# Kernel optimization log

Measured on AMD Instinct MI355X. Metric: run time of the kernel, lower is better.

Reference implementation:

```python
import jax, jax.numpy as jnp
import numpy as np
import math

B, L, NH, HD = 2, 2048, 8, 128
C = NH * HD            # hidden size
K = 3                  # short_conv_L
EMB, ORDER = 33, 64    # hyena filter emb_dim / order


def setup_inputs() -> dict:
    key = jax.random.key(0)
    ks = jax.random.split(key, 10)
    f32 = jnp.float32
    return {
        "query_layer": jax.random.normal(ks[0], (L, B, NH, HD), f32),
        "key_layer": jax.random.normal(ks[1], (L, B, NH, HD), f32),
        "value_layer": jax.random.normal(ks[2], (L, B, NH, HD), f32),
        # depthwise short conv params: [3(qkv), C, 1, K] / [3, C]
        "short_conv_weight": jax.random.normal(ks[3], (3, C, 1, K), f32) * 0.3,
        "short_conv_bias": jax.random.normal(ks[4], (3, C), f32) * 0.02,
        # D term of the long conv, shape [head_dim]
        "long_conv_bias": jax.random.normal(ks[5], (HD,), f32) * 0.1,
        # hyena filter MLP (torch Linear convention: W [out, in])
        "lin0_w": jax.random.normal(ks[6], (ORDER, EMB), f32) * (1.0 / np.sqrt(EMB)),
        "lin0_b": jnp.zeros((ORDER,), f32),
        "lin1_w": jax.random.normal(ks[7], (ORDER, ORDER), f32) * (1.0 / np.sqrt(ORDER)),
        "lin1_b": jnp.zeros((ORDER,), f32),
        "lin2_w": jax.random.normal(ks[8], (ORDER, ORDER), f32) * (1.0 / np.sqrt(ORDER)),
        "lin2_b": jnp.zeros((ORDER,), f32),
        "freq": jnp.ones((1, ORDER), f32),  # Sin activation freq (w=1), shared across layers
        "final_w": jax.random.normal(ks[9], (HD, ORDER), f32) * (1.0 / np.sqrt(ORDER)),
        # exponential modulation decay rates, [1,1,HD], as initialized in the module
        "mod_weight": jnp.linspace(math.log(0.01) / 1.5, math.log(0.01) / 0.3, HD,
                                   dtype=f32)[None, None],
    }


def _depthwise_conv(x, w, b):
    # x [B,C,L], w [C,1,K], b [C]; causal: pad K-1 both sides, keep first L
    y = jax.lax.conv_general_dilated(
        x, w, window_strides=(1,), padding=[(K - 1, K - 1)],
        feature_group_count=C, dimension_numbers=("NCH", "OIH", "NCH"))
    return y[..., :L] + b[None, :, None]


def _hyena_filter(lin0_w, lin0_b, lin1_w, lin1_b, lin2_w, lin2_b, freq, final_w, mod_weight):
    t = jnp.linspace(0.0, 1.0, L)[None, :, None]              # [1,L,1]
    bands = (EMB - 1) // 2
    w_ang = 2.0 * jnp.pi * jnp.linspace(0.0, L - 1.0, L) / L  # [L]
    f = jnp.linspace(1e-4, bands - 1.0, bands)                # [bands]
    theta = w_ang[:, None] * f[None, :]                       # [L,bands]; z = exp(-1j f w)
    z = jnp.concatenate([t[0], jnp.cos(theta), -jnp.sin(theta)], axis=-1)[None]  # [1,L,EMB]
    h = jnp.sin(freq * (z @ lin0_w.T + lin0_b))
    h = jnp.sin(freq * (h @ lin1_w.T + lin1_b))
    h = jnp.sin(freq * (h @ lin2_w.T + lin2_b))
    h = h @ final_w.T                                         # [1,L,HD]
    h = h * jnp.exp(-t * jnp.abs(mod_weight))                 # exponential modulation
    return h[0].T                                             # [HD, L]


def _fftconv_heads(k, kern, D, q, v):
    # mirrors fftconv_heads_ref with head_dim=NH: channels split as (h=HD, d=NH)
    b = k.shape[0]
    kr = k.reshape(b, HD, NH, L).transpose(0, 2, 1, 3)  # b nh hd L  (d1 axis)
    vr = v.reshape(b, HD, NH, L).transpose(0, 2, 1, 3)  # b nh hd L  (d2 axis)
    qr = q.reshape(b, HD, NH, L).transpose(0, 2, 1, 3)  # b nh hd L
    kv = kr[:, :, None] * vr[:, None]                   # [b, nh, nh, hd, L]
    n = 2 * L
    kv_f = jnp.fft.rfft(kv, n=n) / n
    kern_f = jnp.fft.rfft(kern, n=n)                    # [HD, n//2+1]
    y = jnp.fft.irfft(kv_f * kern_f, n=n, norm="forward")[..., :L]
    out = y + kv * D[:, None]                           # D over head_dim axis
    out = (out * qr[:, :, None]).sum(axis=1)            # _mul_sum over d1 -> [b, nh, hd, L]
    return out.transpose(0, 2, 1, 3).reshape(b, C, L)   # 'b d2 h l -> b (h d2) l'


def reference(query_layer, key_layer, value_layer, short_conv_weight, short_conv_bias,
              long_conv_bias, lin0_w, lin0_b, lin1_w, lin1_b, lin2_w, lin2_b,
              freq, final_w, mod_weight):
    # 'sq b np hn -> b (np hn) sq'
    q = jnp.transpose(query_layer, (1, 2, 3, 0)).reshape(B, C, L)
    k = jnp.transpose(key_layer, (1, 2, 3, 0)).reshape(B, C, L)
    v = jnp.transpose(value_layer, (1, 2, 3, 0)).reshape(B, C, L)
    q = _depthwise_conv(q, short_conv_weight[0], short_conv_bias[0])
    k = _depthwise_conv(k, short_conv_weight[1], short_conv_bias[1])
    v = _depthwise_conv(v, short_conv_weight[2], short_conv_bias[2])
    filt = _hyena_filter(lin0_w, lin0_b, lin1_w, lin1_b, lin2_w, lin2_b,
                         freq, final_w, mod_weight)
    # module calls fftconv_heads_ref(k=value, ..., q=query, v=key)
    y = _fftconv_heads(v, filt, long_conv_bias, q=q, v=k)
    # 'b (np hn) sq -> b np sq hn'
    return y.reshape(B, NH, HD, L).transpose(0, 1, 3, 2)
```

## Files before the change

### kernel.cpp

```cpp
#include <hip/hip_runtime.h>
#include <stdint.h>
#include <string.h>

#define L_SEQ 2048
#define B_SZ 2
#define NHH 8
#define HDD 128
#define C_SZ 1024
#define EMB_D 33
#define ORD 64
#define BANDS 16
#define FSTRIDE (L_SEQ + 256)
#define FRS_S 2184
#define FRS_FILL 2176

typedef _Float16 f16;
typedef f16 f16x8 __attribute__((ext_vector_type(8)));
typedef f16 f16x4 __attribute__((ext_vector_type(4)));
typedef float f32x4 __attribute__((ext_vector_type(4)));

__global__ void filter_kernel(const float* __restrict__ w0, const float* __restrict__ b0,
                              const float* __restrict__ w1, const float* __restrict__ b1,
                              const float* __restrict__ w2, const float* __restrict__ b2,
                              const float* __restrict__ fr, const float* __restrict__ wf,
                              const float* __restrict__ md, const float* __restrict__ Dv,
                              float* __restrict__ filt) {
  int tid = threadIdx.x;
  int o = tid & 63;
  int lq = tid >> 6;
  int l = blockIdx.x * 4 + lq;

  if (blockIdx.x < 128) filt[(size_t)blockIdx.x * FSTRIDE + tid] = 0.0f;

  __shared__ float zs[4][EMB_D];
  __shared__ float hs[4][ORD];
  __shared__ float gs[4][ORD];

  float t = (float)l / (float)(L_SEQ - 1);
  float wang = 6.2831853071795864f * (float)l / (float)L_SEQ;
  const float fstep = (15.0f - 1e-4f) / 15.0f;

  if (o == 0) zs[lq][0] = t;
  if (o >= 1 && o < 1 + BANDS) {
    int j = o - 1;
    float fj = 1e-4f + fstep * (float)j;
    zs[lq][1 + j] = cosf(wang * fj);
  }
  if (o >= 1 + BANDS && o < 1 + 2 * BANDS) {
    int j = o - 1 - BANDS;
    float fj = 1e-4f + fstep * (float)j;
    zs[lq][1 + BANDS + j] = -sinf(wang * fj);
  }
  __syncthreads();

  float fo = fr[o];
  float a = b0[o];
  for (int e = 0; e < EMB_D; ++e) a += zs[lq][e] * w0[o * EMB_D + e];
  hs[lq][o] = sinf(fo * a);
  __syncthreads();

  a = b1[o];
  for (int e = 0; e < ORD; ++e) a += hs[lq][e] * w1[o * ORD + e];
  gs[lq][o] = sinf(fo * a);
  __syncthreads();

  a = b2[o];
  for (int e = 0; e < ORD; ++e) a += gs[lq][e] * w2[o * ORD + e];
  float h3 = sinf(fo * a);
  __syncthreads();
  hs[lq][o] = h3;
  __syncthreads();

  #pragma unroll
  for (int pass = 0; pass < 2; ++pass) {
    int hd = pass * 64 + o;
    float acc = 0.0f;
    for (int e = 0; e < ORD; ++e) acc += hs[lq][e] * wf[hd * ORD + e];
    float val = acc * expf(-t * fabsf(md[hd]));
    if (l == 0) val += Dv[hd];
    filt[(size_t)hd * FSTRIDE + 256 + l] = val;
  }
}

#define TLC 64
__global__ void shortconv_kernel(const float* __restrict__ q_in,
                                 const float* __restrict__ k_in,
                                 const float* __restrict__ v_in,
                                 const float* __restrict__ scw,
                                 const float* __restrict__ scb,
                                 float* __restrict__ AqT, f16* __restrict__ Akt16,
                                 f16* __restrict__ Avt16) {
  int bid = blockIdx.x;
  int lt = bid & 31;
  int np = (bid >> 5) & 7;
  int b = bid >> 8;
  int l0 = lt * TLC;
  int tid = threadIdx.x;

  __shared__ float xs[TLC + 2][HDD + 4];
  __shared__ float wcs[HDD][4];

  const float* ins[3] = {q_in, k_in, v_in};

  for (int tsr = 0; tsr < 3; ++tsr) {
    const float* x = ins[tsr];
    if (tid < HDD) {
      int c = np * HDD + tid;
      wcs[tid][0] = scw[(tsr * C_SZ + c) * 3 + 0];
      wcs[tid][1] = scw[(tsr * C_SZ + c) * 3 + 1];
      wcs[tid][2] = scw[(tsr * C_SZ + c) * 3 + 2];
      wcs[tid][3] = scb[tsr * C_SZ + c];
    }
    for (int idx = tid; idx < (TLC + 2) * HDD; idx += 256) {
      int row = idx >> 7, hn = idx & 127;
      int l = l0 - 2 + row;
      float val = 0.0f;
      if (l >= 0) val = x[(((size_t)l * B_SZ + b) * NHH + np) * HDD + hn];
      xs[row][hn] = val;
    }
    __syncthreads();

    int n1 = tid & 7;
    int lp = tid >> 3;
    for (int hdi = 0; hdi < 16; ++hdi) {
      int hn = hdi * 8 + n1;
      float cw0 = wcs[hn][0], cw1 = wcs[hn][1], cw2 = wcs[hn][2], cb = wcs[hn][3];
      int hd = np * 16 + hdi;
      #pragma unroll
      for (int half = 0; half < 2; ++half) {
        int ll = half * 32 + lp;
        float y = cb + cw0 * xs[ll][hn] + cw1 * xs[ll + 1][hn]
                     + cw2 * xs[ll + 2][hn];
        int l = l0 + ll;
        if (tsr == 0) {
          AqT[(((size_t)b * HDD + hd) * NHH + n1) * L_SEQ + l] = y;
        } else {
          int ch = l >> 7, m = l & 127;
          int off = (n1 << 8) | ((m << 1) ^ (n1 << 4));
          char* base = (tsr == 1) ? (char*)Akt16 : (char*)Avt16;
          *(f16*)(base + ((((size_t)(b * HDD + hd)) * 16 + ch) << 11) + off) = (f16)y;
        }
      }
    }
    __syncthreads();
  }
}

__global__ void __launch_bounds__(256, 3)
hyena_main(const float* __restrict__ AqT, const f16* __restrict__ Akt16,
           const f16* __restrict__ Avt16, const float* __restrict__ filt,
           float* __restrict__ out) {
  int bid = blockIdx.x;
  int pr = bid >> 8;
  int hd = bid & 127;
  int b  = (bid >> 7) & 1;
  int tid = threadIdx.x;
  int w = tid >> 6;
  int lane = tid & 63;
  int r = lane & 15;
  int p = lane >> 4;
  int a = (15 - r) & 7;

  const int LT_hi = 15 - pr;
  const int LT_lo = pr;
  const int NCc = 16 - pr;

  __shared__ f16 FRS[8][FRS_S];
  __shared__ f16 AV[4][1024];
  __shared__ f16 AK[4][1024];

  const float* frow = filt + (size_t)hd * FSTRIDE + 256;
  const char* avtg = (const char*)Avt16 + (((size_t)(b * HDD + hd)) * 16 << 11);
  const char* aktg = (const char*)Akt16 + (((size_t)(b * HDD + hd)) * 16 << 11);
  const float* aqtb = AqT + ((size_t)b * HDD + hd) * NHH * L_SEQ;
  int np = hd >> 4, hnb = (hd & 15) * 8;

  for (int aa = 0; aa < 8; ++aa) {
    for (int z4 = tid * 4; z4 < FRS_FILL; z4 += 1024) {
      const float* s = frow + (2044 - aa - z4);
      float4 v;
      __builtin_memcpy(&v, s, 16);
      f16x4 o = {(f16)v.w, (f16)v.z, (f16)v.y, (f16)v.x};
      *(f16x4*)&FRS[aa][z4] = o;
    }
  }

  f32x4 aH[2][4], aL[2][4];
  #pragma unroll
  for (int mi = 0; mi < 2; ++mi)
    #pragma unroll
    for (int nt = 0; nt < 4; ++nt) {
      aH[mi][nt] = f32x4{0.f, 0.f, 0.f, 0.f};
      aL[mi][nt] = f32x4{0.f, 0.f, 0.f, 0.f};
    }

  auto dma = [&](int c, int bi) {
    const char* srcb = (w >> 1) ? aktg : avtg;
    f16* dstb = (w >> 1) ? &AK[bi][(w & 1) * 512] : &AV[bi][(w & 1) * 512];
    const char* src = srcb + ((size_t)c << 11) + (w & 1) * 1024 + lane * 16;
    __builtin_amdgcn_global_load_lds((const unsigned int*)src,
                                     (unsigned int*)dstb, 16, 0, 0);
  };

  auto chunk_body = [&](int c) {
    int bi = c & 3;
    bool do_lo = (c <= LT_lo);
    int zcom = p * 8 - 112 + 16 * (3 - w) - r - a;
    int zbH = 2047 - (LT_hi - c) * 128 + zcom;
    f16x8 fH[6], fL[6];
    #pragma unroll
    for (int j = 0; j < 6; ++j)
      fH[j] = *(const f16x8*)&FRS[a][zbH + 32 * j];
    if (do_lo) {
      int zbL = 2047 - (LT_lo - c) * 128 + zcom;
      #pragma unroll
      for (int j = 0; j < 6; ++j)
        fL[j] = *(const f16x8*)&FRS[a][zbL + 32 * j];
    }
    int ky = r & 7;
    __builtin_amdgcn_s_setprio(1);
    #pragma unroll
    for (int s = 0; s < 4; ++s) {
      f16x8 kf = *(const f16x8*)&AK[bi][ky * 128 + ((s * 32 + p * 8) ^ (ky * 8))];
      #pragma unroll
      for (int nt = 0; nt < 4; ++nt) {
        int vy = nt * 2 + (r >> 3);
        f16x8 vf = *(const f16x8*)&AV[bi][vy * 128 + ((s * 32 + p * 8) ^ (vy * 8))];
        f16x8 bf = vf * kf;
        aH[0][nt] = __builtin_amdgcn_mfma_f32_16x16x32_f16(
            fH[s + 2], bf, aH[0][nt], 0, 0, 0);
        aH[1][nt] = __builtin_amdgcn_mfma_f32_16x16x32_f16(
            fH[s], bf, aH[1][nt], 0, 0, 0);
        if (do_lo) {
          aL[0][nt] = __builtin_amdgcn_mfma_f32_16x16x32_f16(
              fL[s + 2], bf, aL[0][nt], 0, 0, 0);
          aL[1][nt] = __builtin_amdgcn_mfma_f32_16x16x32_f16(
              fL[s], bf, aL[1][nt], 0, 0, 0);
        }
      }
    }
    __builtin_amdgcn_s_setprio(0);
  };

  auto epilogue = [&](int lt, f32x4 (&acc)[2][4]) {
    int l0 = lt * 128;
    int hi = r >> 3;
    int n2 = r & 7;
    #pragma unroll
    for (int mi = 0; mi < 2; ++mi) {
      int mt = w + 4 * mi;
      float4 qv[4];
      #pragma unroll
      for (int nt = 0; nt < 4; ++nt)
        qv[nt] = *(const float4*)(aqtb + (size_t)(nt * 2 + hi) * L_SEQ
                                  + l0 + mt * 16 + p * 4);
      #pragma unroll
      for (int reg = 0; reg < 4; ++reg) {
        float pv = qv[0][reg] * acc[mi][0][reg] + qv[1][reg] * acc[mi][1][reg]
                 + qv[2][reg] * acc[mi][2][reg] + qv[3][reg] * acc[mi][3][reg];
        pv += __shfl_xor(pv, 8, 64);
        if (r < 8) {
          int i = mt * 16 + p * 4 + reg;
          out[(((size_t)b * NHH + np) * L_SEQ + (l0 + i)) * HDD + hnb + n2] = pv;
        }
      }
    }
  };

  dma(0, 0); dma(1, 1);

  int iters = (NCc + 1) >> 1;
  for (int it = 0; it < iters; ++it) {
    int c0 = 2 * it, c1 = 2 * it + 1;
    asm volatile("s_waitcnt vmcnt(0) lgkmcnt(0)" ::: "memory");
    __builtin_amdgcn_s_barrier();
    __builtin_amdgcn_sched_barrier(0);
    if (c0 + 2 < NCc) dma(c0 + 2, (c0 + 2) & 3);
    if (c1 + 2 < NCc) dma(c1 + 2, (c1 + 2) & 3);
    chunk_body(c0);
    if (c1 < NCc) chunk_body(c1);
  }

  epilogue(LT_hi, aH);
  epilogue(LT_lo, aL);
}

extern "C" void kernel_launch(void* const* d_in, const int* in_sizes, int n_in,
                              void* d_out, int out_size, void* d_ws, size_t ws_size,
                              hipStream_t stream) {
  const float* q_in = (const float*)d_in[0];
  const float* k_in = (const float*)d_in[1];
  const float* v_in = (const float*)d_in[2];
  const float* scw  = (const float*)d_in[3];
  const float* scb  = (const float*)d_in[4];
  const float* Dv   = (const float*)d_in[5];
  const float* w0   = (const float*)d_in[6];
  const float* b0   = (const float*)d_in[7];
  const float* w1   = (const float*)d_in[8];
  const float* b1   = (const float*)d_in[9];
  const float* w2   = (const float*)d_in[10];
  const float* b2   = (const float*)d_in[11];
  const float* fr   = (const float*)d_in[12];
  const float* wf   = (const float*)d_in[13];
  const float* md   = (const float*)d_in[14];

  float* ws   = (float*)d_ws;
  float* filt = ws;
  float* AqT  = ws + (size_t)HDD * FSTRIDE;
  f16*   Akt16 = (f16*)(AqT + (size_t)B_SZ * HDD * L_SEQ * NHH);
  f16*   Avt16 = Akt16 + (size_t)B_SZ * HDD * 16 * 1024;

  filter_kernel<<<512, 256, 0, stream>>>(w0, b0, w1, b1, w2, b2, fr, wf, md, Dv, filt);
  shortconv_kernel<<<512, 256, 0, stream>>>(q_in, k_in, v_in, scw, scb, AqT, Akt16, Avt16);
  hyena_main<<<2048, 256, 0, stream>>>(AqT, Akt16, Avt16, filt, (float*)d_out);
}
```

Baseline: 146.6 us.

## Precompute MFMA filter fragments in global memory and store q in fp16

Adds an afrag_prep kernel that reverses each filter row to fp16 and lays out per-lane MFMA A-fragments in a global buffer. hyena_main then loads these fragments directly from global/L2 instead of building an 8-way shifted Toeplitz copy in shared memory per block. This removes a large per-block LDS fill and frees about 35KB of LDS, which may allow higher occupancy. The q operand is also stored as fp16, halving epilogue reads at some precision cost, and fragment loads now hit global memory inside the inner loop.

```diff
diff --git a/kernel.cpp b/kernel.cpp
--- a/kernel.cpp
+++ b/kernel.cpp
@@ -11,8 +11,7 @@
 #define ORD 64
 #define BANDS 16
 #define FSTRIDE (L_SEQ + 256)
-#define FRS_S 2184
-#define FRS_FILL 2176
+#define NSI 134
 
 typedef _Float16 f16;
 typedef f16 f16x8 __attribute__((ext_vector_type(8)));
@@ -82,13 +81,32 @@
   }
 }
 
+__global__ void afrag_prep(const float* __restrict__ filt, f16* __restrict__ G) {
+  int hd = blockIdx.x;
+  int tid = threadIdx.x;
+  __shared__ f16 frevs[2304];
+  const float* row = filt + (size_t)hd * FSTRIDE;
+  for (int x = tid; x < 2304; x += 256) frevs[x] = (f16)row[2303 - x];
+  __syncthreads();
+  f16* gh = G + (size_t)hd * NSI * 64 * 8;
+  for (int t = tid; t < NSI * 64; t += 256) {
+    int si = t >> 6, lane = t & 63;
+    int r = lane & 15, p = lane >> 4;
+    int S = 16 * si + 8 * p - r + 15;
+    f16x8 v;
+    #pragma unroll
+    for (int i = 0; i < 8; ++i) v[i] = frevs[S + i];
+    *(f16x8*)(gh + (size_t)t * 8) = v;
+  }
+}
+
 #define TLC 64
 __global__ void shortconv_kernel(const float* __restrict__ q_in,
                                  const float* __restrict__ k_in,
                                  const float* __restrict__ v_in,
                                  const float* __restrict__ scw,
                                  const float* __restrict__ scb,
-                                 float* __restrict__ AqT, f16* __restrict__ Akt16,
+                                 f16* __restrict__ AqT16, f16* __restrict__ Akt16,
                                  f16* __restrict__ Avt16) {
   int bid = blockIdx.x;
   int lt = bid & 31;
@@ -133,7 +151,7 @@
                      + cw2 * xs[ll + 2][hn];
         int l = l0 + ll;
         if (tsr == 0) {
-          AqT[(((size_t)b * HDD + hd) * NHH + n1) * L_SEQ + l] = y;
+          AqT16[(((size_t)b * HDD + hd) * NHH + n1) * L_SEQ + l] = (f16)y;
         } else {
           int ch = l >> 7, m = l & 127;
           int off = (n1 << 8) | ((m << 1) ^ (n1 << 4));
@@ -147,8 +165,8 @@
 }
 
 __global__ void __launch_bounds__(256, 3)
-hyena_main(const float* __restrict__ AqT, const f16* __restrict__ Akt16,
-           const f16* __restrict__ Avt16, const float* __restrict__ filt,
+hyena_main(const f16* __restrict__ AqT16, const f16* __restrict__ Akt16,
+           const f16* __restrict__ Avt16, const f16* __restrict__ G,
            float* __restrict__ out) {
   int bid = blockIdx.x;
   int pr = bid >> 8;
@@ -159,31 +177,19 @@
   int lane = tid & 63;
   int r = lane & 15;
   int p = lane >> 4;
-  int a = (15 - r) & 7;
 
   const int LT_hi = 15 - pr;
   const int LT_lo = pr;
   const int NCc = 16 - pr;
 
-  __shared__ f16 FRS[8][FRS_S];
   __shared__ f16 AV[4][1024];
   __shared__ f16 AK[4][1024];
 
-  const float* frow = filt + (size_t)hd * FSTRIDE + 256;
   const char* avtg = (const char*)Avt16 + (((size_t)(b * HDD + hd)) * 16 << 11);
   const char* aktg = (const char*)Akt16 + (((size_t)(b * HDD + hd)) * 16 << 11);
-  const float* aqtb = AqT + ((size_t)b * HDD + hd) * NHH * L_SEQ;
+  const f16* aqtb = AqT16 + ((size_t)b * HDD + hd) * NHH * L_SEQ;
+  const f16* gl = G + ((size_t)hd * NSI * 64 + lane) * 8;
   int np = hd >> 4, hnb = (hd & 15) * 8;
-
-  for (int aa = 0; aa < 8; ++aa) {
-    for (int z4 = tid * 4; z4 < FRS_FILL; z4 += 1024) {
-      const float* s = frow + (2044 - aa - z4);
-      float4 v;
-      __builtin_memcpy(&v, s, 16);
-      f16x4 o = {(f16)v.w, (f16)v.z, (f16)v.y, (f16)v.x};
-      *(f16x4*)&FRS[aa][z4] = o;
-    }
-  }
 
   f32x4 aH[2][4], aL[2][4];
   #pragma unroll
@@ -205,17 +211,16 @@
   auto chunk_body = [&](int c) {
     int bi = c & 3;
     bool do_lo = (c <= LT_lo);
-    int zcom = p * 8 - 112 + 16 * (3 - w) - r - a;
-    int zbH = 2047 - (LT_hi - c) * 128 + zcom;
+    int siH0 = 123 - w - 8 * (LT_hi - c);
     f16x8 fH[6], fL[6];
     #pragma unroll
     for (int j = 0; j < 6; ++j)
-      fH[j] = *(const f16x8*)&FRS[a][zbH + 32 * j];
+      fH[j] = *(const f16x8*)(gl + (size_t)(siH0 + 2 * j) * 512);
     if (do_lo) {
-      int zbL = 2047 - (LT_lo - c) * 128 + zcom;
+      int siL0 = 123 - w - 8 * (LT_lo - c);
       #pragma unroll
       for (int j = 0; j < 6; ++j)
-        fL[j] = *(const f16x8*)&FRS[a][zbL + 32 * j];
+        fL[j] = *(const f16x8*)(gl + (size_t)(siL0 + 2 * j) * 512);
     }
     int ky = r & 7;
     __builtin_amdgcn_s_setprio(1);
@@ -249,15 +254,17 @@
     #pragma unroll
     for (int mi = 0; mi < 2; ++mi) {
       int mt = w + 4 * mi;
-      float4 qv[4];
+      f16x4 qh[4];
       #pragma unroll
       for (int nt = 0; nt < 4; ++nt)
-        qv[nt] = *(const float4*)(aqtb + (size_t)(nt * 2 + hi) * L_SEQ
-                                  + l0 + mt * 16 + p * 4);
+        qh[nt] = *(const f16x4*)(aqtb + (size_t)(nt * 2 + hi) * L_SEQ
+                                 + l0 + mt * 16 + p * 4);
       #pragma unroll
       for (int reg = 0; reg < 4; ++reg) {
-        float pv = qv[0][reg] * acc[mi][0][reg] + qv[1][reg] * acc[mi][1][reg]
-                 + qv[2][reg] * acc[mi][2][reg] + qv[3][reg] * acc[mi][3][reg];
+        float pv = (float)qh[0][reg] * acc[mi][0][reg]
+                 + (float)qh[1][reg] * acc[mi][1][reg]
+                 + (float)qh[2][reg] * acc[mi][2][reg]
+                 + (float)qh[3][reg] * acc[mi][3][reg];
         pv += __shfl_xor(pv, 8, 64);
         if (r < 8) {
           int i = mt * 16 + p * 4 + reg;
@@ -304,13 +311,15 @@
   const float* wf   = (const float*)d_in[13];
   const float* md   = (const float*)d_in[14];
 
-  float* ws   = (float*)d_ws;
-  float* filt = ws;
-  float* AqT  = ws + (size_t)HDD * FSTRIDE;
-  f16*   Akt16 = (f16*)(AqT + (size_t)B_SZ * HDD * L_SEQ * NHH);
-  f16*   Avt16 = Akt16 + (size_t)B_SZ * HDD * 16 * 1024;
+  float* ws    = (float*)d_ws;
+  float* filt  = ws;
+  f16* AqT16   = (f16*)(ws + (size_t)HDD * FSTRIDE);
+  f16* Akt16   = AqT16 + (size_t)B_SZ * HDD * NHH * L_SEQ;
+  f16* Avt16   = Akt16 + (size_t)B_SZ * HDD * 16 * 1024;
+  f16* Gfrag   = Avt16 + (size_t)B_SZ * HDD * 16 * 1024;
 
   filter_kernel<<<512, 256, 0, stream>>>(w0, b0, w1, b1, w2, b2, fr, wf, md, Dv, filt);
-  shortconv_kernel<<<512, 256, 0, stream>>>(q_in, k_in, v_in, scw, scb, AqT, Akt16, Avt16);
-  hyena_main<<<2048, 256, 0, stream>>>(AqT, Akt16, Avt16, filt, (float*)d_out);
-}
+  afrag_prep<<<128, 256, 0, stream>>>(filt, Gfrag);
+  shortconv_kernel<<<512, 256, 0, stream>>>(q_in, k_in, v_in, scw, scb, AqT16, Akt16, Avt16);
+  hyena_main<<<2048, 256, 0, stream>>>(AqT16, Akt16, Avt16, Gfrag, (float*)d_out);
+}
```

New measurement: 322.1 us. 2.2x slower.
